# Optimization experiments

Measured on AMD Instinct MI355X. Metric: run time of the kernel, lower is better.

Reference implementation:

```python
import jax, jax.numpy as jnp
import numpy as np

B, S, H_SZ = 1, 2048, 2048
E, K, KVH, D = 8, 2, 16, 128      # experts, top_k, kv heads, head_dim
QH = K * KVH                       # 32 query heads
QSZ = KVH * D                      # 2048 per-expert q/o size


def setup_inputs() -> dict:
    key = jax.random.key(0)
    ks = jax.random.split(key, 6)
    hidden_states = jax.random.normal(ks[0], (B, S, H_SZ), jnp.float32)
    causal = jnp.tril(jnp.ones((S, S), dtype=bool))
    attention_bias = jnp.where(causal, 0.0, -1e9).astype(jnp.float32)[None, None]  # [1,1,S,S]
    inv_freq = 1.0 / (10000.0 ** (jnp.arange(0, D, 2, dtype=jnp.float32) / D))     # [D/2]
    ang = jnp.arange(S, dtype=jnp.float32)[:, None] * inv_freq[None, :]            # [S,D/2]
    cos, sin = jnp.cos(ang), jnp.sin(ang)
    router_w = jax.random.normal(ks[1], (E, H_SZ), jnp.float32) * 0.02
    q_w = jax.random.normal(ks[2], (E, QSZ, H_SZ), jnp.float32) * 0.02
    o_w = jax.random.normal(ks[3], (E, H_SZ, QSZ), jnp.float32) * 0.02
    kv_w = jax.random.normal(ks[4], (2 * QSZ, H_SZ), jnp.float32) * 0.02
    bias = jax.random.normal(ks[5], (H_SZ,), jnp.float32) * 0.02
    return {"hidden_states": hidden_states, "attention_bias": attention_bias,
            "cos": cos, "sin": sin, "router_w": router_w, "q_w": q_w,
            "o_w": o_w, "kv_w": kv_w, "bias": bias}


def _rope(x, cos, sin):
    # x: [b,s,h,d]; half-rotation rotary, cos/sin: [s,d/2]
    d2 = x.shape[-1] // 2
    x1, x2 = x[..., :d2], x[..., d2:]
    c = cos[None, :, None, :]
    s = sin[None, :, None, :]
    return jnp.concatenate([x1 * c - x2 * s, x1 * s + x2 * c], axis=-1)


def reference(hidden_states, attention_bias, cos, sin, router_w, q_w, o_w, kv_w, bias):
    # ---- router: top-k + softmax over top-k logits ----
    logits = jnp.einsum('bsh,eh->bse', hidden_states, router_w)         # [b,s,E]
    top_vals, sel = jax.lax.top_k(logits, K)                            # [b,s,K]
    gates = jax.nn.softmax(top_vals, axis=-1)                           # [b,s,K]
    # ---- per-expert Q projections (dense, as in original), gather selected ----
    q_all = jnp.einsum('bsh,eqh->bseq', hidden_states, q_w)             # [b,s,E,QSZ]
    q_sel = jnp.take_along_axis(q_all, sel[..., None], axis=2)          # [b,s,K,QSZ]
    # slots -> kv-major head layout: [b,s,K,KVH,D] -> [b,s,KVH,K,D] -> [b,s,QH,D]
    q = q_sel.reshape(B, S, K, KVH, D).transpose(0, 1, 3, 2, 4).reshape(B, S, QH, D)
    # ---- shared K/V ----
    kv = jnp.einsum('bsh,oh->bso', hidden_states, kv_w)                 # [b,s,2*QSZ]
    k_st, v_st = jnp.split(kv, 2, axis=-1)
    k_st = k_st.reshape(B, S, KVH, D)
    v_st = v_st.reshape(B, S, KVH, D)
    # ---- rotary ----
    q = _rope(q, cos, sin)
    k_st = _rope(k_st, cos, sin)
    # ---- GQA attention (group size K; kv-major query layout matches repeat) ----
    k_rep = jnp.repeat(k_st, K, axis=2)                                 # [b,s,QH,D]
    v_rep = jnp.repeat(v_st, K, axis=2)
    scale = D ** -0.5
    scores = jnp.einsum('bqhd,bkhd->bhqk', q, k_rep) * scale + attention_bias
    probs = jax.nn.softmax(scores, axis=-1)
    attn = jnp.einsum('bhqk,bkhd->bqhd', probs, v_rep)                  # [b,s,QH,D]
    # back to slot-major: [b,s,KVH,K,D] -> [b,s,K,KVH,D] -> [b,s,K,QSZ]
    attn4 = attn.reshape(B, S, KVH, K, D).transpose(0, 1, 3, 2, 4).reshape(B, S, K, QSZ)
    # ---- per-expert O projections, masked + gated sum (as in original) ----
    out = jnp.zeros((B, S, H_SZ), hidden_states.dtype)
    for e in range(E):
        o_e = jnp.einsum('bskq,hq->bskh', attn4, o_w[e])                # [b,s,K,H]
        m = (sel == e).astype(hidden_states.dtype) * gates              # [b,s,K]
        out = out + jnp.einsum('bsk,bskh->bsh', m, o_e)
    return out + bias
```

## Files before the change

kernel.cpp:

```cpp
#include <hip/hip_runtime.h>
#include <hip/hip_bf16.h>
#include <stdint.h>

#define S_LEN 2048
#define HSZ 2048
#define NE 8
#define TOPK 2
#define NKVH 16
#define HD 128
#define NQH 32
#define QSZ 2048

typedef __attribute__((ext_vector_type(8))) __bf16 bf16x8;
typedef __attribute__((ext_vector_type(4))) float f32x4;

#define BM 128
#define BN 128
#define BK 32

__device__ __forceinline__ void gload_lds16(const void* g, void* l) {
  __builtin_amdgcn_global_load_lds((__attribute__((address_space(1))) void*)g,
                                   (__attribute__((address_space(3))) void*)l, 16, 0, 0);
}

__device__ __forceinline__ bf16x8 pack8(float4 a, float4 b) {
  bf16x8 r;
  r[0] = (__bf16)a.x; r[1] = (__bf16)a.y; r[2] = (__bf16)a.z; r[3] = (__bf16)a.w;
  r[4] = (__bf16)b.x; r[5] = (__bf16)b.y; r[6] = (__bf16)b.z; r[7] = (__bf16)b.w;
  return r;
}

__global__ __launch_bounds__(256) void cast_kernel(const float* __restrict__ src,
                                                   __bf16* __restrict__ dst, long n) {
  long i0 = ((long)blockIdx.x * 256 + threadIdx.x) * 4;
  long stride = (long)gridDim.x * 256 * 4;
  for (long i = i0; i < n; i += stride) {
    float4 v = *(const float4*)(src + i);
    unsigned short a = __builtin_bit_cast(unsigned short, (__bf16)v.x);
    unsigned short b = __builtin_bit_cast(unsigned short, (__bf16)v.y);
    unsigned short c = __builtin_bit_cast(unsigned short, (__bf16)v.z);
    unsigned short d = __builtin_bit_cast(unsigned short, (__bf16)v.w);
    uint2 o;
    o.x = (unsigned)a | ((unsigned)b << 16);
    o.y = (unsigned)c | ((unsigned)d << 16);
    *(uint2*)(dst + i) = o;
  }
}

__global__ __launch_bounds__(256) void router_kernel(const float* __restrict__ hs,
                                                     const float* __restrict__ rw,
                                                     int* __restrict__ sel,
                                                     float* __restrict__ gates) {
  const int s = blockIdx.x * 4 + (threadIdx.x >> 6);
  const int lane = threadIdx.x & 63;
  const float* row = hs + (size_t)s * HSZ;
  float acc[NE];
#pragma unroll
  for (int e = 0; e < NE; ++e) acc[e] = 0.f;
  for (int j = lane; j < HSZ; j += 64) {
    float x = row[j];
#pragma unroll
    for (int e = 0; e < NE; ++e) acc[e] += x * rw[e * HSZ + j];
  }
#pragma unroll
  for (int e = 0; e < NE; ++e) {
#pragma unroll
    for (int off = 32; off > 0; off >>= 1) acc[e] += __shfl_xor(acc[e], off);
  }
  if (lane == 0) {
    int i0 = 0; float v0 = acc[0];
#pragma unroll
    for (int e = 1; e < NE; ++e) if (acc[e] > v0) { v0 = acc[e]; i0 = e; }
    int i1 = -1; float v1 = -1e30f;
#pragma unroll
    for (int e = 0; e < NE; ++e) if (e != i0 && acc[e] > v1) { v1 = acc[e]; i1 = e; }
    float ge = __expf(v1 - v0);
    float den = 1.f + ge;
    sel[s * 2] = i0; sel[s * 2 + 1] = i1;
    gates[s * 2] = 1.f / den; gates[s * 2 + 1] = ge / den;
  }
}

__global__ void bucket_kernel(const int* __restrict__ sel, int* __restrict__ pair_list,
                              int* __restrict__ expert_off) {
  __shared__ int cnt[NE], base[NE];
  const int t = threadIdx.x;
  if (t < NE) cnt[t] = 0;
  __syncthreads();
  for (int p2 = t; p2 < S_LEN * TOPK; p2 += 256) atomicAdd(&cnt[sel[p2]], 1);
  __syncthreads();
  if (t == 0) {
    int run = 0;
#pragma unroll
    for (int e = 0; e < NE; ++e) { base[e] = run; expert_off[e] = run; run += cnt[e]; }
    expert_off[NE] = run;
  }
  __syncthreads();
  for (int p2 = t; p2 < S_LEN * TOPK; p2 += 256) {
    int pos = atomicAdd(&base[sel[p2]], 1);
    pair_list[pos] = p2;
  }
}

template <int MODE>
__global__ __launch_bounds__(256, 4) void gemm_kernel(
    const __bf16* __restrict__ A_src, const float* __restrict__ B_src,
    const int* __restrict__ pair_list, const int* __restrict__ expert_off,
    const float* __restrict__ gates, __bf16* __restrict__ out0,
    __bf16* __restrict__ out_vT) {
  constexpr int KD = 2048;
  constexpr int NT = (MODE == 0) ? 64 : 32;
  const int n0 = blockIdx.x * BN;
  const int m0 = blockIdx.y * BM;
  int kbase = 0, kz = 0, start = 0, cntv = S_LEN;
  const float* Bb = B_src;
  if constexpr (MODE != 0) {
    const int e = blockIdx.z >> 1;
    kz = blockIdx.z & 1;
    kbase = kz * 1024;
    start = expert_off[e];
    cntv = expert_off[e + 1] - start;
    if (m0 >= cntv) return;
    Bb = B_src + (size_t)e * QSZ * HSZ;
  }
  __shared__ __attribute__((aligned(16))) __bf16 As[2][BM * BK];
  __shared__ __attribute__((aligned(16))) __bf16 Bs[2][BN * BK];
  __shared__ const __bf16* a_rows[BM];
  __shared__ int row_pair[BM];
  const int t = threadIdx.x;
  if (t < BM) {
    if constexpr (MODE == 0) {
      a_rows[t] = A_src + (size_t)(m0 + t) * KD;
      row_pair[t] = 0;
    } else {
      int idx = m0 + t;
      bool valid = idx < cntv;
      int pp = pair_list[start + (valid ? idx : 0)];
      row_pair[t] = valid ? pp : -1;
      size_t arow = (MODE == 1) ? (size_t)(pp >> 1) : (size_t)pp;
      a_rows[t] = A_src + arow * (size_t)KD + kbase;
    }
  }
  __syncthreads();

  const int lane = t & 63, w = t >> 6;
  const int wr = (w >> 1) * 64, wc = (w & 1) * 64;
  const int lr = lane & 15, g = lane >> 4;

  const __bf16* a_srow[2];
  int a_scol[2];
#pragma unroll
  for (int i = 0; i < 2; ++i) {
    const int c = t + i * 256;
    a_srow[i] = a_rows[c >> 2];
    a_scol[i] = (c & 3) * 8;
  }

  const float* bp = Bb + (size_t)(n0 + (t >> 1)) * KD + kbase + (t & 1) * 16;
  const int bwo = (t >> 1) * BK + (t & 1) * 16;

  f32x4 acc[4][4];
#pragma unroll
  for (int m = 0; m < 4; ++m)
#pragma unroll
    for (int n = 0; n < 4; ++n) acc[m][n] = (f32x4)0.f;

  auto stageA = [&](int buf, int k0) {
#pragma unroll
    for (int i = 0; i < 2; ++i)
      gload_lds16(a_srow[i] + k0 + a_scol[i], (char*)As[buf] + (t + i * 256) * 16);
  };

  float4 c0, c1, c2, c3;
#define B_LOAD(KB)                                                           \
  c0 = *(const float4*)(bp + (KB));     c1 = *(const float4*)(bp + (KB) + 4); \
  c2 = *(const float4*)(bp + (KB) + 8); c3 = *(const float4*)(bp + (KB) + 12);

  stageA(0, 0);
  B_LOAD(0)
  __builtin_amdgcn_sched_barrier(0);

#pragma unroll 2
  for (int ti = 0; ti < NT; ++ti) {
    const int cur = ti & 1;
    *(bf16x8*)(&Bs[cur][bwo]) = pack8(c0, c1);
    *(bf16x8*)(&Bs[cur][bwo + 8]) = pack8(c2, c3);
    asm volatile("s_waitcnt lgkmcnt(0)" ::: "memory");
    __builtin_amdgcn_s_barrier();
    __builtin_amdgcn_sched_barrier(0);
    if (ti + 1 < NT) {
      stageA(cur ^ 1, (ti + 1) * BK);
      B_LOAD((ti + 1) * BK)
    }
    __builtin_amdgcn_sched_barrier(0);
    {
      bf16x8 af[4], bfv[4];
#pragma unroll
      for (int m = 0; m < 4; ++m)
        af[m] = *(const bf16x8*)(&As[cur][(wr + m * 16 + lr) * BK + g * 8]);
#pragma unroll
      for (int n = 0; n < 4; ++n)
        bfv[n] = *(const bf16x8*)(&Bs[cur][(wc + n * 16 + lr) * BK + g * 8]);
#pragma unroll
      for (int m = 0; m < 4; ++m)
#pragma unroll
        for (int n = 0; n < 4; ++n)
          acc[m][n] = __builtin_amdgcn_mfma_f32_16x16x32_bf16(af[m], bfv[n], acc[m][n], 0, 0, 0);
    }
    __builtin_amdgcn_sched_barrier(0);
  }
#undef B_LOAD

  const int lg = lane >> 4;
  if constexpr (MODE == 0) {
    if (n0 < 2048) {
#pragma unroll
      for (int m = 0; m < 4; ++m)
#pragma unroll
        for (int r = 0; r < 4; ++r) {
          const int row = wr + m * 16 + lg * 4 + r;
#pragma unroll
          for (int n = 0; n < 4; ++n) {
            const int col = n0 + wc + n * 16 + lr;
            out0[(size_t)(m0 + row) * 2048 + col] = (__bf16)acc[m][n][r];
          }
        }
    } else {
#pragma unroll
      for (int m = 0; m < 4; ++m) {
        const int sb = m0 + wr + m * 16 + lg * 4;
#pragma unroll
        for (int n = 0; n < 4; ++n) {
          const int cv = n0 + wc + n * 16 + lr - 2048;
          uint2 pk;
          unsigned short h0 = __builtin_bit_cast(unsigned short, (__bf16)acc[m][n][0]);
          unsigned short h1 = __builtin_bit_cast(unsigned short, (__bf16)acc[m][n][1]);
          unsigned short h2 = __builtin_bit_cast(unsigned short, (__bf16)acc[m][n][2]);
          unsigned short h3 = __builtin_bit_cast(unsigned short, (__bf16)acc[m][n][3]);
          pk.x = (unsigned)h0 | ((unsigned)h1 << 16);
          pk.y = (unsigned)h2 | ((unsigned)h3 << 16);
          *(uint2*)(out_vT + (size_t)cv * S_LEN + sb) = pk;
        }
      }
    }
  } else {
    __bf16* outp = out0 + (size_t)kz * 4096 * 2048;
#pragma unroll
    for (int m = 0; m < 4; ++m) {
#pragma unroll
      for (int r = 0; r < 4; ++r) {
        const int row = wr + m * 16 + lg * 4 + r;
        const int pp = row_pair[row];
        if (pp < 0) continue;
        float gt = 1.f;
        if constexpr (MODE == 2) gt = gates[pp];
#pragma unroll
        for (int n = 0; n < 4; ++n) {
          const int col = n0 + wc + n * 16 + lr;
          outp[(size_t)pp * 2048 + col] = (__bf16)(acc[m][n][r] * gt);
        }
      }
    }
  }
}

__global__ __launch_bounds__(256) void rope_k_kernel(const __bf16* __restrict__ kv_lin,
                                                     const float* __restrict__ cosb,
                                                     const float* __restrict__ sinb,
                                                     __bf16* __restrict__ k_attn) {
  const int idx = blockIdx.x * 4 + (threadIdx.x >> 6);
  const int lane = threadIdx.x & 63;
  const int s = idx >> 4;
  const int gq = idx & 15;
  const __bf16* ksrc = kv_lin + (size_t)s * 2048 + gq * HD;
  float x1 = (float)ksrc[lane], x2 = (float)ksrc[lane + 64];
  float c = cosb[s * 64 + lane], sn = sinb[s * 64 + lane];
  __bf16* kd = k_attn + ((size_t)gq * S_LEN + s) * HD;
  kd[lane] = (__bf16)(x1 * c - x2 * sn);
  kd[lane + 64] = (__bf16)(x1 * sn + x2 * c);
}

__global__ __launch_bounds__(256, 2) void attn_kernel(const __bf16* __restrict__ q_part,
                                                      const __bf16* __restrict__ k_attn,
                                                      const __bf16* __restrict__ vT,
                                                      const float* __restrict__ cosb,
                                                      const float* __restrict__ sinb,
                                                      __bf16* __restrict__ attn4) {
  __shared__ __attribute__((aligned(16))) __bf16 Ks[2][64 * 128];
  __shared__ __attribute__((aligned(16))) __bf16 Vs[2][128 * 64];
  const int h = blockIdx.x;
  const int by = (blockIdx.y < 8) ? blockIdx.y : 23 - blockIdx.y;
  const int s0 = by * 128;
  const int t = threadIdx.x;
  const int lane = t & 63;
  const int w = t >> 6;
  const int g = lane >> 4;
  const int lr = lane & 15;
  const int kvh = h >> 1;

  int koff[4], voff[4];
#pragma unroll
  for (int i = 0; i < 4; ++i) {
    const int c = t + i * 256;
    const int kvL = c >> 4, w16 = c & 15;
    koff[i] = kvL * HD + ((w16 ^ (kvL & 7)) * 8);
    const int d = c >> 3, w8 = c & 7;
    voff[i] = d * S_LEN + ((w8 ^ (d & 7)) * 8);
  }
  const __bf16* Kb = k_attn + (size_t)kvh * S_LEN * HD;
  const __bf16* Vb = vT + (size_t)kvh * HD * S_LEN;

  auto stage = [&](int buf, int kv0) {
#pragma unroll
    for (int i = 0; i < 4; ++i) {
      const int c = t + i * 256;
      gload_lds16(Kb + (size_t)kv0 * HD + koff[i], (char*)Ks[buf] + c * 16);
      gload_lds16(Vb + (size_t)kv0 + voff[i], (char*)Vs[buf] + c * 16);
    }
  };

  bf16x8 qf[2][4];
#pragma unroll
  for (int m = 0; m < 2; ++m) {
    const int qrow = s0 + w * 32 + m * 16 + lr;
    const __bf16* p0 = q_part + (size_t)(qrow * 2 + (h & 1)) * QSZ + kvh * HD;
    const __bf16* p1 = p0 + (size_t)4096 * 2048;
    const float* cp = cosb + qrow * 64;
    const float* sp = sinb + qrow * 64;
#pragma unroll
    for (int ds = 0; ds < 4; ++ds) {
      const int d0 = ds * 32 + g * 8;
      const int dl = d0 & 63;
      const bf16x8 xa = *(const bf16x8*)(p0 + d0);
      const bf16x8 xb = *(const bf16x8*)(p1 + d0);
      const bf16x8 ya = *(const bf16x8*)(p0 + (d0 ^ 64));
      const bf16x8 yb = *(const bf16x8*)(p1 + (d0 ^ 64));
      bf16x8 o;
#pragma unroll
      for (int j = 0; j < 8; ++j) {
        const float x = (float)xa[j] + (float)xb[j];
        const float y = (float)ya[j] + (float)yb[j];
        const float c = cp[dl + j], sn = sp[dl + j];
        o[j] = (__bf16)((ds < 2) ? (x * c - y * sn) : (y * sn + x * c));
      }
      qf[m][ds] = o;
    }
  }

  float m_run[2] = {-1e30f, -1e30f}, l_run[2] = {0.f, 0.f};
  f32x4 acc[2][8];
#pragma unroll
  for (int m = 0; m < 2; ++m)
#pragma unroll
    for (int dt = 0; dt < 8; ++dt) acc[m][dt] = (f32x4)0.f;

  const int xr = (lr & 7) << 4;
  const int nt = 2 * by + 2;
  stage(0, 0);
  for (int ti = 0; ti < nt; ++ti) {
    const int cur = ti & 1;
    const int kv0 = ti * 64;
    __syncthreads();
    if (ti + 1 < nt) stage(cur ^ 1, kv0 + 64);

    f32x4 sc[2][4];
#pragma unroll
    for (int m = 0; m < 2; ++m)
#pragma unroll
      for (int b = 0; b < 4; ++b) sc[m][b] = (f32x4)0.f;
#pragma unroll
    for (int b = 0; b < 4; ++b) {
#pragma unroll
      for (int ds = 0; ds < 4; ++ds) {
        const bf16x8 kf = *(const bf16x8*)((const char*)Ks[cur] +
            (b * 16 + lr) * 256 + ((ds * 64 + g * 16) ^ xr));
        sc[0][b] = __builtin_amdgcn_mfma_f32_16x16x32_bf16(kf, qf[0][ds], sc[0][b], 0, 0, 0);
        sc[1][b] = __builtin_amdgcn_mfma_f32_16x16x32_bf16(kf, qf[1][ds], sc[1][b], 0, 0, 0);
      }
    }

    bf16x8 paf[2][2];
#pragma unroll
    for (int m = 0; m < 2; ++m) {
      const int qrow = s0 + w * 32 + m * 16 + lr;
      float p[4][4];
      float tmax = -1e30f;
#pragma unroll
      for (int b = 0; b < 4; ++b)
#pragma unroll
        for (int r = 0; r < 4; ++r) {
          const int kv = kv0 + b * 16 + g * 4 + r;
          float v = sc[m][b][r] * 0.08838834764831845f;
          if (kv > qrow) v = -1e30f;
          p[b][r] = v;
          tmax = fmaxf(tmax, v);
        }
      tmax = fmaxf(tmax, __shfl_xor(tmax, 16));
      tmax = fmaxf(tmax, __shfl_xor(tmax, 32));
      const float m_new = fmaxf(m_run[m], tmax);
      const float alpha = __expf(m_run[m] - m_new);
      float lsum = 0.f;
#pragma unroll
      for (int b = 0; b < 4; ++b)
#pragma unroll
        for (int r = 0; r < 4; ++r) {
          p[b][r] = __expf(p[b][r] - m_new);
          lsum += p[b][r];
        }
      lsum += __shfl_xor(lsum, 16);
      lsum += __shfl_xor(lsum, 32);
      l_run[m] = l_run[m] * alpha + lsum;
      m_run[m] = m_new;

      float ar[4];
#pragma unroll
      for (int r = 0; r < 4; ++r) ar[r] = __shfl(alpha, g * 4 + r);
#pragma unroll
      for (int dt = 0; dt < 8; ++dt)
#pragma unroll
        for (int r = 0; r < 4; ++r) acc[m][dt][r] *= ar[r];

#pragma unroll
      for (int half = 0; half < 2; ++half) {
        bf16x8 af;
#pragma unroll
        for (int j = 0; j < 8; ++j) {
          const int srcl = lr + 16 * ((g & 1) * 2 + (j >> 2));
          const float va = __shfl(p[half * 2][j & 3], srcl);
          const float vb = __shfl(p[half * 2 + 1][j & 3], srcl);
          af[j] = (__bf16)((g >> 1) ? vb : va);
        }
        paf[m][half] = af;
      }
    }

#pragma unroll
    for (int dt = 0; dt < 8; ++dt) {
      const char* vrow = (const char*)Vs[cur] + (dt * 16 + lr) * 128;
      const bf16x8 v0 = *(const bf16x8*)(vrow + ((g * 16) ^ xr));
      const bf16x8 v1 = *(const bf16x8*)(vrow + ((64 + g * 16) ^ xr));
      acc[0][dt] = __builtin_amdgcn_mfma_f32_16x16x32_bf16(paf[0][0], v0, acc[0][dt], 0, 0, 0);
      acc[0][dt] = __builtin_amdgcn_mfma_f32_16x16x32_bf16(paf[0][1], v1, acc[0][dt], 0, 0, 0);
      acc[1][dt] = __builtin_amdgcn_mfma_f32_16x16x32_bf16(paf[1][0], v0, acc[1][dt], 0, 0, 0);
      acc[1][dt] = __builtin_amdgcn_mfma_f32_16x16x32_bf16(paf[1][1], v1, acc[1][dt], 0, 0, 0);
    }
  }

#pragma unroll
  for (int m = 0; m < 2; ++m) {
    const float li = 1.f / l_run[m];
    float linv[4];
#pragma unroll
    for (int r = 0; r < 4; ++r) linv[r] = __shfl(li, g * 4 + r);
#pragma unroll
    for (int dt = 0; dt < 8; ++dt)
#pragma unroll
      for (int r = 0; r < 4; ++r) {
        const int qg = s0 + w * 32 + m * 16 + g * 4 + r;
        attn4[((size_t)qg * 2 + (h & 1)) * QSZ + kvh * HD + dt * 16 + lr] =
            (__bf16)(acc[m][dt][r] * linv[r]);
      }
  }
}

__global__ __launch_bounds__(256) void final_kernel(const __bf16* __restrict__ o_part,
                                                    const float* __restrict__ bias,
                                                    float* __restrict__ out) {
  const size_t i = ((size_t)blockIdx.x * 256 + threadIdx.x) * 4;
  const int s = (int)(i >> 11);
  const int hcol = (int)(i & 2047);
  float4 r = *(const float4*)(bias + hcol);
#pragma unroll
  for (int idx = 0; idx < 4; ++idx) {
    const size_t row = (size_t)(idx >> 1) * 4096 + 2 * s + (idx & 1);
    const ushort4 u = *(const ushort4*)(o_part + row * HSZ + hcol);
    r.x += (float)__builtin_bit_cast(__bf16, u.x);
    r.y += (float)__builtin_bit_cast(__bf16, u.y);
    r.z += (float)__builtin_bit_cast(__bf16, u.z);
    r.w += (float)__builtin_bit_cast(__bf16, u.w);
  }
  *(float4*)(out + i) = r;
}

extern "C" void kernel_launch(void* const* d_in, const int* in_sizes, int n_in,
                              void* d_out, int out_size, void* d_ws, size_t ws_size,
                              hipStream_t stream) {
  (void)in_sizes; (void)n_in; (void)out_size; (void)ws_size;
  const float* hs = (const float*)d_in[0];
  const float* cosb = (const float*)d_in[2];
  const float* sinb = (const float*)d_in[3];
  const float* rw = (const float*)d_in[4];
  const float* qw = (const float*)d_in[5];
  const float* ow = (const float*)d_in[6];
  const float* kvw = (const float*)d_in[7];
  const float* bias = (const float*)d_in[8];
  float* outp = (float*)d_out;

  char* base = (char*)d_ws;
  size_t off = 0;
  auto take = [&](size_t bytes) {
    char* r = base + off;
    off += (bytes + 255) & ~(size_t)255;
    return r;
  };
  __bf16* hid_bf  = (__bf16*)take((size_t)S_LEN * HSZ * 2);
  __bf16* k_attn  = (__bf16*)take((size_t)NKVH * S_LEN * HD * 2);
  __bf16* v_attnT = (__bf16*)take((size_t)NKVH * HD * S_LEN * 2);
  char* bufA = take((size_t)S_LEN * 4096 * 2);
  char* bufBC = take((size_t)2 * 4096 * HSZ * 2);
  int* sel = (int*)take((size_t)S_LEN * TOPK * 4);
  float* gates = (float*)take((size_t)S_LEN * TOPK * 4);
  int* pair_list = (int*)take((size_t)S_LEN * TOPK * 4);
  int* expert_off = (int*)take((size_t)(NE + 1) * 4);

  __bf16* kv_lin = (__bf16*)bufA;
  __bf16* attn4 = (__bf16*)bufA;
  __bf16* q_part = (__bf16*)bufBC;
  __bf16* o_part = (__bf16*)bufBC;

  cast_kernel<<<1024, 256, 0, stream>>>(hs, hid_bf, (long)S_LEN * HSZ);
  router_kernel<<<S_LEN / 4, 256, 0, stream>>>(hs, rw, sel, gates);
  bucket_kernel<<<1, 256, 0, stream>>>(sel, pair_list, expert_off);
  gemm_kernel<0><<<dim3(4096 / BN, S_LEN / BM, 1), 256, 0, stream>>>(
      hid_bf, kvw, nullptr, nullptr, nullptr, kv_lin, v_attnT);
  rope_k_kernel<<<S_LEN * NKVH / 4, 256, 0, stream>>>(kv_lin, cosb, sinb, k_attn);
  gemm_kernel<1><<<dim3(QSZ / BN, 16, NE * 2), 256, 0, stream>>>(
      hid_bf, qw, pair_list, expert_off, nullptr, q_part, nullptr);
  attn_kernel<<<dim3(NQH, 16), 256, 0, stream>>>(q_part, k_attn, v_attnT, cosb, sinb, attn4);
  gemm_kernel<2><<<dim3(HSZ / BN, 16, NE * 2), 256, 0, stream>>>(
      attn4, ow, pair_list, expert_off, gates, o_part, nullptr);
  final_kernel<<<(S_LEN * HSZ / 4) / 256, 256, 0, stream>>>(o_part, bias, outp);
}
```

Before: 431.7 us.

## Pre-cast weights to bf16 and use larger swizzled async-LDS GEMM tiles

Adds a new GEMM path, used when the workspace is large enough. The fp32 q, o and kv weights are first cast to bf16 buffers in the workspace on every call. A new 512-thread GEMM then streams both A and B straight into LDS with global_load_lds, using XOR-swizzled layouts and larger 128/256x256x64 tiles. The aim is to drop the repeated fp32 weight reads and per-tile in-register conversion, and to raise MFMA work per block. The cost is extra cast kernels that read and write roughly 450 MB per call. The new kernel also runs at one block per CU, so overlap depends on double buffering within the block.

```diff
diff --git a/kernel.cpp b/kernel.cpp
--- a/kernel.cpp
+++ b/kernel.cpp
@@ -13,10 +13,6 @@
 
 typedef __attribute__((ext_vector_type(8))) __bf16 bf16x8;
 typedef __attribute__((ext_vector_type(4))) float f32x4;
-
-#define BM 128
-#define BN 128
-#define BK 32
 
 __device__ __forceinline__ void gload_lds16(const void* g, void* l) {
   __builtin_amdgcn_global_load_lds((__attribute__((address_space(1))) void*)g,
@@ -102,6 +98,175 @@
   }
 }
 
+template <int MODE>
+__global__ __launch_bounds__(512, 1) void gemm12_kernel(
+    const __bf16* __restrict__ A_src, const __bf16* __restrict__ B_src,
+    const int* __restrict__ pair_list, const int* __restrict__ expert_off,
+    const float* __restrict__ gates, __bf16* __restrict__ out0,
+    __bf16* __restrict__ out_vT) {
+  constexpr int KD = 2048;
+  constexpr int TBM = (MODE == 0) ? 128 : 256;
+  constexpr int TBN = 256;
+  constexpr int TBK = 64;
+  constexpr int NT = ((MODE == 0) ? KD : KD / 2) / TBK;
+  constexpr int CA = TBM * 8 / 512;
+  constexpr int MF = (MODE == 0) ? 4 : 8;
+  const int n0 = blockIdx.x * TBN;
+  const int m0 = blockIdx.y * TBM;
+  int kbase = 0, kz = 0, start = 0, cntv = S_LEN;
+  const __bf16* Bb = B_src;
+  if constexpr (MODE != 0) {
+    const int e = blockIdx.z >> 1;
+    kz = blockIdx.z & 1;
+    kbase = kz * 1024;
+    start = expert_off[e];
+    cntv = expert_off[e + 1] - start;
+    if (m0 >= cntv) return;
+    Bb = B_src + (size_t)e * QSZ * HSZ;
+  }
+  __shared__ __attribute__((aligned(16))) __bf16 As[2][TBM * TBK];
+  __shared__ __attribute__((aligned(16))) __bf16 Bs[2][TBN * TBK];
+  __shared__ const __bf16* a_rows[TBM];
+  __shared__ int row_pair[TBM];
+  const int t = threadIdx.x;
+  if (t < TBM) {
+    if constexpr (MODE == 0) {
+      a_rows[t] = A_src + (size_t)(m0 + t) * KD;
+      row_pair[t] = 0;
+    } else {
+      int idx = m0 + t;
+      bool valid = idx < cntv;
+      int pp = pair_list[start + (valid ? idx : 0)];
+      row_pair[t] = valid ? pp : -1;
+      size_t arow = (MODE == 1) ? (size_t)(pp >> 1) : (size_t)pp;
+      a_rows[t] = A_src + arow * (size_t)KD + kbase;
+    }
+  }
+  __syncthreads();
+
+  const int lane = t & 63, w = t >> 6;
+  const int wr = (w >> 2) * (TBM / 2), wc = (w & 3) * 64;
+  const int lr = lane & 15, g = lane >> 4;
+  const int xa = lr & 7;
+
+  const __bf16* a_srow[CA];
+  int a_soff[CA];
+#pragma unroll
+  for (int i = 0; i < CA; ++i) {
+    const int c = t + i * 512;
+    const int row = c >> 3, win = c & 7;
+    a_srow[i] = a_rows[row];
+    a_soff[i] = (win ^ (row & 7)) * 8;
+  }
+  const __bf16* b_srow[4];
+  int b_soff[4];
+#pragma unroll
+  for (int i = 0; i < 4; ++i) {
+    const int c = t + i * 512;
+    const int row = c >> 3, win = c & 7;
+    b_srow[i] = Bb + (size_t)(n0 + row) * KD + kbase;
+    b_soff[i] = (win ^ (row & 7)) * 8;
+  }
+
+  auto stage = [&](int buf, int k0) {
+#pragma unroll
+    for (int i = 0; i < CA; ++i)
+      gload_lds16(a_srow[i] + k0 + a_soff[i], (char*)As[buf] + (t + i * 512) * 16);
+#pragma unroll
+    for (int i = 0; i < 4; ++i)
+      gload_lds16(b_srow[i] + k0 + b_soff[i], (char*)Bs[buf] + (t + i * 512) * 16);
+  };
+
+  f32x4 acc[MF][4];
+#pragma unroll
+  for (int m = 0; m < MF; ++m)
+#pragma unroll
+    for (int n = 0; n < 4; ++n) acc[m][n] = (f32x4)0.f;
+
+  stage(0, 0);
+  asm volatile("s_waitcnt vmcnt(0)" ::: "memory");
+  __builtin_amdgcn_s_barrier();
+
+  for (int ti = 0; ti < NT; ++ti) {
+    const int cur = ti & 1;
+    if (ti + 1 < NT) stage(cur ^ 1, (ti + 1) * TBK);
+    __builtin_amdgcn_sched_barrier(0);
+#pragma unroll
+    for (int kk = 0; kk < TBK; kk += 32) {
+      bf16x8 af[MF], bfv[4];
+#pragma unroll
+      for (int m = 0; m < MF; ++m)
+        af[m] = *(const bf16x8*)(&As[cur][(wr + m * 16 + lr) * TBK + (((kk >> 3) + g) ^ xa) * 8]);
+#pragma unroll
+      for (int n = 0; n < 4; ++n)
+        bfv[n] = *(const bf16x8*)(&Bs[cur][(wc + n * 16 + lr) * TBK + (((kk >> 3) + g) ^ xa) * 8]);
+#pragma unroll
+      for (int m = 0; m < MF; ++m)
+#pragma unroll
+        for (int n = 0; n < 4; ++n)
+          acc[m][n] = __builtin_amdgcn_mfma_f32_16x16x32_bf16(af[m], bfv[n], acc[m][n], 0, 0, 0);
+    }
+    __builtin_amdgcn_sched_barrier(0);
+    asm volatile("s_waitcnt vmcnt(0)" ::: "memory");
+    __builtin_amdgcn_s_barrier();
+  }
+
+  const int lg = lane >> 4;
+  if constexpr (MODE == 0) {
+    if (n0 < 2048) {
+#pragma unroll
+      for (int m = 0; m < MF; ++m)
+#pragma unroll
+        for (int r = 0; r < 4; ++r) {
+          const int row = wr + m * 16 + lg * 4 + r;
+#pragma unroll
+          for (int n = 0; n < 4; ++n) {
+            const int col = n0 + wc + n * 16 + lr;
+            out0[(size_t)(m0 + row) * 2048 + col] = (__bf16)acc[m][n][r];
+          }
+        }
+    } else {
+#pragma unroll
+      for (int m = 0; m < MF; ++m) {
+        const int sb = m0 + wr + m * 16 + lg * 4;
+#pragma unroll
+        for (int n = 0; n < 4; ++n) {
+          const int cv = n0 + wc + n * 16 + lr - 2048;
+          uint2 pk;
+          unsigned short h0 = __builtin_bit_cast(unsigned short, (__bf16)acc[m][n][0]);
+          unsigned short h1 = __builtin_bit_cast(unsigned short, (__bf16)acc[m][n][1]);
+          unsigned short h2 = __builtin_bit_cast(unsigned short, (__bf16)acc[m][n][2]);
+          unsigned short h3 = __builtin_bit_cast(unsigned short, (__bf16)acc[m][n][3]);
+          pk.x = (unsigned)h0 | ((unsigned)h1 << 16);
+          pk.y = (unsigned)h2 | ((unsigned)h3 << 16);
+          *(uint2*)(out_vT + (size_t)cv * S_LEN + sb) = pk;
+        }
+      }
+    }
+  } else {
+    __bf16* outp = out0 + (size_t)kz * 4096 * 2048;
+#pragma unroll
+    for (int m = 0; m < MF; ++m) {
+#pragma unroll
+      for (int r = 0; r < 4; ++r) {
+        const int row = wr + m * 16 + lg * 4 + r;
+        const int pp = row_pair[row];
+        if (pp < 0) continue;
+        float gt = 1.f;
+        if constexpr (MODE == 2) gt = gates[pp];
+#pragma unroll
+        for (int n = 0; n < 4; ++n) {
+          const int col = n0 + wc + n * 16 + lr;
+          outp[(size_t)pp * 2048 + col] = (__bf16)(acc[m][n][r] * gt);
+        }
+      }
+    }
+  }
+}
+
+#define BM 128
+#define BN 128
+#define BK 32
 template <int MODE>
 __global__ __launch_bounds__(256, 4) void gemm_kernel(
     const __bf16* __restrict__ A_src, const float* __restrict__ B_src,
@@ -142,11 +307,9 @@
     }
   }
   __syncthreads();
-
   const int lane = t & 63, w = t >> 6;
   const int wr = (w >> 1) * 64, wc = (w & 1) * 64;
   const int lr = lane & 15, g = lane >> 4;
-
   const __bf16* a_srow[2];
   int a_scol[2];
 #pragma unroll
@@ -155,31 +318,25 @@
     a_srow[i] = a_rows[c >> 2];
     a_scol[i] = (c & 3) * 8;
   }
-
   const float* bp = Bb + (size_t)(n0 + (t >> 1)) * KD + kbase + (t & 1) * 16;
   const int bwo = (t >> 1) * BK + (t & 1) * 16;
-
   f32x4 acc[4][4];
 #pragma unroll
   for (int m = 0; m < 4; ++m)
 #pragma unroll
     for (int n = 0; n < 4; ++n) acc[m][n] = (f32x4)0.f;
-
   auto stageA = [&](int buf, int k0) {
 #pragma unroll
     for (int i = 0; i < 2; ++i)
       gload_lds16(a_srow[i] + k0 + a_scol[i], (char*)As[buf] + (t + i * 256) * 16);
   };
-
   float4 c0, c1, c2, c3;
 #define B_LOAD(KB)                                                           \
   c0 = *(const float4*)(bp + (KB));     c1 = *(const float4*)(bp + (KB) + 4); \
   c2 = *(const float4*)(bp + (KB) + 8); c3 = *(const float4*)(bp + (KB) + 12);
-
   stageA(0, 0);
   B_LOAD(0)
   __builtin_amdgcn_sched_barrier(0);
-
 #pragma unroll 2
   for (int ti = 0; ti < NT; ++ti) {
     const int cur = ti & 1;
@@ -210,7 +367,6 @@
     __builtin_amdgcn_sched_barrier(0);
   }
 #undef B_LOAD
-
   const int lg = lane >> 4;
   if constexpr (MODE == 0) {
     if (n0 < 2048) {
@@ -485,7 +641,7 @@
 extern "C" void kernel_launch(void* const* d_in, const int* in_sizes, int n_in,
                               void* d_out, int out_size, void* d_ws, size_t ws_size,
                               hipStream_t stream) {
-  (void)in_sizes; (void)n_in; (void)out_size; (void)ws_size;
+  (void)in_sizes; (void)n_in; (void)out_size;
   const float* hs = (const float*)d_in[0];
   const float* cosb = (const float*)d_in[2];
   const float* sinb = (const float*)d_in[3];
@@ -512,6 +668,10 @@
   float* gates = (float*)take((size_t)S_LEN * TOPK * 4);
   int* pair_list = (int*)take((size_t)S_LEN * TOPK * 4);
   int* expert_off = (int*)take((size_t)(NE + 1) * 4);
+  __bf16* qw_bf  = (__bf16*)take((size_t)NE * QSZ * HSZ * 2);
+  __bf16* ow_bf  = (__bf16*)take((size_t)NE * HSZ * QSZ * 2);
+  __bf16* kvw_bf = (__bf16*)take((size_t)2 * QSZ * HSZ * 2);
+  const bool wide = ws_size >= off;
 
   __bf16* kv_lin = (__bf16*)bufA;
   __bf16* attn4 = (__bf16*)bufA;
@@ -521,13 +681,28 @@
   cast_kernel<<<1024, 256, 0, stream>>>(hs, hid_bf, (long)S_LEN * HSZ);
   router_kernel<<<S_LEN / 4, 256, 0, stream>>>(hs, rw, sel, gates);
   bucket_kernel<<<1, 256, 0, stream>>>(sel, pair_list, expert_off);
-  gemm_kernel<0><<<dim3(4096 / BN, S_LEN / BM, 1), 256, 0, stream>>>(
-      hid_bf, kvw, nullptr, nullptr, nullptr, kv_lin, v_attnT);
-  rope_k_kernel<<<S_LEN * NKVH / 4, 256, 0, stream>>>(kv_lin, cosb, sinb, k_attn);
-  gemm_kernel<1><<<dim3(QSZ / BN, 16, NE * 2), 256, 0, stream>>>(
-      hid_bf, qw, pair_list, expert_off, nullptr, q_part, nullptr);
-  attn_kernel<<<dim3(NQH, 16), 256, 0, stream>>>(q_part, k_attn, v_attnT, cosb, sinb, attn4);
-  gemm_kernel<2><<<dim3(HSZ / BN, 16, NE * 2), 256, 0, stream>>>(
-      attn4, ow, pair_list, expert_off, gates, o_part, nullptr);
+
+  if (wide) {
+    cast_kernel<<<2048, 256, 0, stream>>>(qw, qw_bf, (long)NE * QSZ * HSZ);
+    cast_kernel<<<2048, 256, 0, stream>>>(ow, ow_bf, (long)NE * HSZ * QSZ);
+    cast_kernel<<<1024, 256, 0, stream>>>(kvw, kvw_bf, (long)2 * QSZ * HSZ);
+    gemm12_kernel<0><<<dim3(4096 / 256, S_LEN / 128, 1), 512, 0, stream>>>(
+        hid_bf, kvw_bf, nullptr, nullptr, nullptr, kv_lin, v_attnT);
+    rope_k_kernel<<<S_LEN * NKVH / 4, 256, 0, stream>>>(kv_lin, cosb, sinb, k_attn);
+    gemm12_kernel<1><<<dim3(QSZ / 256, 8, NE * 2), 512, 0, stream>>>(
+        hid_bf, qw_bf, pair_list, expert_off, nullptr, q_part, nullptr);
+    attn_kernel<<<dim3(NQH, 16), 256, 0, stream>>>(q_part, k_attn, v_attnT, cosb, sinb, attn4);
+    gemm12_kernel<2><<<dim3(HSZ / 256, 8, NE * 2), 512, 0, stream>>>(
+        attn4, ow_bf, pair_list, expert_off, gates, o_part, nullptr);
+  } else {
+    gemm_kernel<0><<<dim3(4096 / BN, S_LEN / BM, 1), 256, 0, stream>>>(
+        hid_bf, kvw, nullptr, nullptr, nullptr, kv_lin, v_attnT);
+    rope_k_kernel<<<S_LEN * NKVH / 4, 256, 0, stream>>>(kv_lin, cosb, sinb, k_attn);
+    gemm_kernel<1><<<dim3(QSZ / BN, 16, NE * 2), 256, 0, stream>>>(
+        hid_bf, qw, pair_list, expert_off, nullptr, q_part, nullptr);
+    attn_kernel<<<dim3(NQH, 16), 256, 0, stream>>>(q_part, k_attn, v_attnT, cosb, sinb, attn4);
+    gemm_kernel<2><<<dim3(HSZ / BN, 16, NE * 2), 256, 0, stream>>>(
+        attn4, ow, pair_list, expert_off, gates, o_part, nullptr);
+  }
   final_kernel<<<(S_LEN * HSZ / 4) / 256, 256, 0, stream>>>(o_part, bias, outp);
 }
```

Measured after the change: 461.2 us. 1.07x slower.
